# Optimization experiments

Hardware: AMD Instinct MI355X
Metric: run time of the kernel (lower is better)

## Reference

```python
import jax, jax.numpy as jnp
import numpy as np

SR = 8                      # search_range
MO = 2 * SR + 1             # max_offset = 17
NC = MO * MO                # 289 cost-volume channels


def _l2_normalize(x, eps=1e-12):
    # torch F.normalize(p=2, dim=1): x / max(||x||_2, eps)
    n = jnp.sqrt(jnp.sum(x * x, axis=1, keepdims=True))
    return x / jnp.maximum(n, eps)


def _conv2d(x, w, b, pad, groups=1):
    out = jax.lax.conv_general_dilated(
        x, w, window_strides=(1, 1), padding=[(pad, pad), (pad, pad)],
        feature_group_count=groups,
        dimension_numbers=('NCHW', 'OIHW', 'NCHW'))
    return out + b[None, :, None, None]


def _cost_volume(x1, x2, sr, norm_both=False):
    x1 = _l2_normalize(x1)
    if norm_both:
        x2 = _l2_normalize(x2)
    bs, c, h, w = x1.shape
    padded = jnp.pad(x2, ((0, 0), (0, 0), (sr, sr), (sr, sr)))
    mo = 2 * sr + 1
    # offsets in (j outer, i inner) order, matching the original double loop
    jj, ii = jnp.meshgrid(jnp.arange(mo), jnp.arange(mo), indexing='ij')
    offs = jnp.stack([jj.reshape(-1), ii.reshape(-1)], axis=-1)  # [mo^2, 2]

    def step(carry, off):
        sl = jax.lax.dynamic_slice(padded, (0, 0, off[0], off[1]), (bs, c, h, w))
        return carry, jnp.mean(x1 * sl, axis=1)  # [bs, h, w]

    _, cv = jax.lax.scan(step, None, offs)       # [mo^2, bs, h, w]
    cv = jnp.transpose(cv, (1, 0, 2, 3))          # [bs, mo^2, h, w]
    return jax.nn.leaky_relu(cv, 0.1)


def setup_inputs() -> dict:
    key = jax.random.key(0)
    ks = jax.random.split(key, 8)
    bs, c, h, w = 4, 256, 64, 64
    scale = 0.05
    return {
        'f1': jax.random.normal(ks[0], (bs, c, h, w), jnp.float32),
        'f2': jax.random.normal(ks[1], (bs, c, h, w), jnp.float32),
        'att_w': jax.random.normal(ks[2], (NC, 1, 7, 7), jnp.float32) * scale,
        'att_b': jax.random.normal(ks[3], (NC,), jnp.float32) * scale,
        'agg1_w': jax.random.normal(ks[4], (NC // 2, NC, 3, 3), jnp.float32) * scale,
        'agg1_b': jax.random.normal(ks[5], (NC // 2,), jnp.float32) * scale,
        'agg2_w': jax.random.normal(ks[6], (49, NC // 2, 3, 3), jnp.float32) * scale,
        'agg2_b': jax.random.normal(ks[7], (49,), jnp.float32) * scale,
    }


def reference(f1, f2, att_w, att_b, agg1_w, agg1_b, agg2_w, agg2_b):
    match_vol = _cost_volume(f1, f2, SR, norm_both=False)          # [bs,289,h,w]
    att = _conv2d(match_vol, att_w, att_b, pad=3, groups=NC)       # depthwise 7x7
    att_vol = match_vol * att
    h1 = jax.nn.relu(_conv2d(att_vol, agg1_w, agg1_b, pad=1))      # Conv(289->144,3)
    out = jax.nn.relu(_conv2d(h1, agg2_w, agg2_b, pad=1))          # Conv(144->49,3)
    return out
```

## Files before the change

kernel.cpp:

```cpp
#include <hip/hip_runtime.h>
#include <hip/hip_bf16.h>

#define BS   4
#define C    256
#define HW   4096
#define NPIX 16384
#define NCH  289
#define MO   17
#define PH   80
#define PW   80
#define C1   144
#define C2   49
#define ASTR 264
#define ICP  320
#define IC3  192
#define CVP  70
#define CVC  320
#define CH64 72

typedef __bf16  bf16x8 __attribute__((ext_vector_type(8)));
typedef float   f32x4  __attribute__((ext_vector_type(4)));
typedef unsigned short us8 __attribute__((ext_vector_type(8)));

__device__ __forceinline__ void halo_zero_dev(unsigned short* p, int H, int halo,
                                              int Cc, int blk, int t) {
    int W = H;
    int inter = H - 2 * halo;
    int total_pos = H * W - inter * inter;
    int chunks = Cc >> 3;
    size_t tot = (size_t)total_pos * chunks * BS;
    size_t idx = (size_t)blk * 256 + t;
    if (idx >= tot) return;
    int c8 = (int)(idx % chunks);
    size_t r = idx / chunks;
    int pos = (int)(r % total_pos);
    int b = (int)(r / total_pos);
    int h, w;
    int topbot = 2 * halo * W;
    if (pos < halo * W) { h = pos / W; w = pos % W; }
    else if (pos < topbot) { int q = pos - halo * W; h = H - halo + q / W; w = q % W; }
    else {
        int q = pos - topbot;
        int row = q / (2 * halo), off = q % (2 * halo);
        h = halo + row;
        w = (off < halo) ? off : (W - 2 * halo + off);
    }
    us8 z = {0, 0, 0, 0, 0, 0, 0, 0};
    *(us8*)&p[(((size_t)b * H + h) * W + w) * Cc + c8 * 8] = z;
}

__global__ void setup_kernel(unsigned short* __restrict__ x2bf, unsigned short* __restrict__ cvp,
                             unsigned short* __restrict__ avp, unsigned short* __restrict__ h1p,
                             const float* __restrict__ w1, unsigned short* __restrict__ wb1,
                             const float* __restrict__ w2, unsigned short* __restrict__ wb2,
                             const float* __restrict__ att_w, float* __restrict__ wdwp,
                             const float* __restrict__ f1, unsigned short* __restrict__ x1bf,
                             const float* __restrict__ f2) {
    __shared__ float shmem[16 * 257 + 16];
    int blk = blockIdx.x;
    int t = threadIdx.x;
    if (blk < 4030) {
        if (blk < 1152) { halo_zero_dev(x2bf, PH, 8, C, blk, t); return; }
        if (blk < 1655) { halo_zero_dev(cvp, CVP, 3, CVC, blk - 1152, t); return; }
        if (blk < 1818) { halo_zero_dev(avp, 66, 1, ICP, blk - 1655, t); return; }
        if (blk < 1916) { halo_zero_dev(h1p, 66, 1, IC3, blk - 1818, t); return; }
        if (blk < 3536) {
            int idx = (blk - 1916) * 256 + t;
            int tap = idx / (C1 * ICP);
            int r = idx - tap * (C1 * ICP);
            int oc = r / ICP;
            int ic = r - oc * ICP;
            float v = (ic < NCH) ? w1[((size_t)(oc * NCH + ic)) * 9 + tap] : 0.f;
            __hip_bfloat16 hb = __float2bfloat16(v);
            wb1[idx] = *(unsigned short*)&hb;
            return;
        }
        if (blk < 3968) {
            int idx = (blk - 3536) * 256 + t;
            int tap = idx / (64 * IC3);
            int r = idx - tap * (64 * IC3);
            int oc = r / IC3;
            int ic = r - oc * IC3;
            float v = (oc < C2 && ic < C1) ? w2[((size_t)(oc * C1 + ic)) * 9 + tap] : 0.f;
            __hip_bfloat16 hb = __float2bfloat16(v);
            wb2[idx] = *(unsigned short*)&hb;
            return;
        }
        {
            int idx = (blk - 3968) * 256 + t;
            if (idx >= 49 * CVC) return;
            int tap = idx / CVC;
            int ch = idx - tap * CVC;
            wdwp[idx] = (ch < NCH) ? att_w[ch * 49 + tap] : 0.f;
        }
        return;
    }
    if (blk < 5054) {
        float* tileT = shmem;
        float* invS = shmem + 16 * 257;
        int bb = blk - 4030;
        int pblk = bb & 255, b = bb >> 8;
        int p0 = pblk * 16;
        int tx = t & 15, ty = t >> 4;
        const float* s = f1 + (size_t)b * C * HW;
#pragma unroll
        for (int i2 = 0; i2 < 16; ++i2) {
            int c = ty + 16 * i2;
            tileT[tx * 257 + c] = s[(size_t)c * HW + p0 + tx];
        }
        __syncthreads();
        int px = t >> 4;
        int l = t & 15;
        float ssum = 0.f;
#pragma unroll
        for (int j2 = 0; j2 < 16; ++j2) {
            float v = tileT[px * 257 + l + 16 * j2];
            ssum += v * v;
        }
        ssum += __shfl_xor(ssum, 1);
        ssum += __shfl_xor(ssum, 2);
        ssum += __shfl_xor(ssum, 4);
        ssum += __shfl_xor(ssum, 8);
        if (l == 0) invS[px] = 1.0f / fmaxf(sqrtf(ssum), 1e-12f);
        __syncthreads();
#pragma unroll 4
        for (int p = 0; p < 16; ++p) {
            float v = tileT[p * 257 + t] * invS[p];
            __hip_bfloat16 hb = __float2bfloat16(v);
            x1bf[((size_t)b * HW + p0 + p) * C + t] = *(unsigned short*)&hb;
        }
        return;
    }
    {
        float* tile = shmem;
        int bb = blk - 5054;
        int pblk = bb & 127;
        int cblk = (bb >> 7) & 7;
        int b    = bb >> 10;
        int tx = t & 31, ty = t >> 5;
        int c0 = cblk * 32, p0 = pblk * 32;
        const float* s = f2 + (size_t)b * C * HW;
#pragma unroll
        for (int i = 0; i < 4; ++i) {
            int c = c0 + ty + 8 * i;
            tile[(ty + 8 * i) * 33 + tx] = s[(size_t)c * HW + p0 + tx];
        }
        __syncthreads();
#pragma unroll
        for (int i = 0; i < 4; ++i) {
            int p = p0 + ty + 8 * i;
            float v = tile[tx * 33 + ty + 8 * i];
            int c = c0 + tx;
            int h = p >> 6, w = p & 63;
            __hip_bfloat16 hb = __float2bfloat16(v);
            x2bf[(((size_t)b * PH + h + 8) * PW + (w + 8)) * C + c] = *(unsigned short*)&hb;
        }
    }
}

__global__ __launch_bounds__(512, 2)
void cv_mfma_kernel(const unsigned short* __restrict__ x1b,
                    const unsigned short* __restrict__ x2b,
                    unsigned short* __restrict__ cvp) {
    __shared__ __align__(16) unsigned short x2s[2][32 * ASTR];
    int i = blockIdx.x;
    int xcd = i & 7;
    int j = i >> 3;
    int hp = xcd * 2 + (j & 1);
    int jj = j >> 1;
    int wseg = jj & 3;
    int b = jj >> 2;
    int h0 = hp * 4;
    int w0 = wseg * 16;
    int t = threadIdx.x;
    int wave = t >> 6, lane = t & 63;
    int lrow = lane & 15, quad = lane >> 4;
    int row_w = wave >> 1, ct = wave & 1;
    int h = h0 + row_w;
    int col_l = ct * 16 + lrow;

    const unsigned short* x1p = x1b + ((size_t)b * HW + h * 64 + w0) * C;
    bf16x8 a[8];
#pragma unroll
    for (int kk = 0; kk < 8; ++kk)
        a[kk] = *(const bf16x8*)&x1p[(size_t)lrow * C + kk * 32 + quad * 8];

    const unsigned short* x2base = x2b + (size_t)b * PH * PW * C;

    {
        const unsigned short* rowp = x2base + ((size_t)h0 * PW + w0) * C;
#pragma unroll
        for (int s = 0; s < 2; ++s) {
            int v = t + s * 512;
            int col = v >> 5, ch8 = v & 31;
            *(us8*)&x2s[0][col * ASTR + ch8 * 8] = *(const us8*)&rowp[(size_t)col * C + ch8 * 8];
        }
    }
    __syncthreads();

    for (int rr = 0; rr < 20; ++rr) {
        us8 pr[2];
        bool dop = (rr + 1 < 20);
        if (dop) {
            const unsigned short* rowp = x2base + ((size_t)(h0 + rr + 1) * PW + w0) * C;
#pragma unroll
            for (int s = 0; s < 2; ++s) {
                int v = t + s * 512;
                int col = v >> 5, ch8 = v & 31;
                pr[s] = *(const us8*)&rowp[(size_t)col * C + ch8 * 8];
            }
        }

        int dj = rr - row_w;
        if ((unsigned)dj <= 16u) {
            const unsigned short* xs = x2s[rr & 1];
            f32x4 acc = {0.f, 0.f, 0.f, 0.f};
#pragma unroll
            for (int kk = 0; kk < 8; ++kk) {
                bf16x8 bb = *(const bf16x8*)&xs[col_l * ASTR + kk * 32 + quad * 8];
                acc = __builtin_amdgcn_mfma_f32_16x16x32_bf16(a[kk], bb, acc, 0, 0, 0);
            }
#pragma unroll
            for (int r = 0; r < 4; ++r) {
                int px_l = quad * 4 + r;
                int di = col_l - px_l;
                if ((unsigned)di <= 16u) {
                    float v = acc[r] * (1.0f / 256.0f);
                    v = (v > 0.f) ? v : 0.1f * v;
                    __hip_bfloat16 hb = __float2bfloat16(v);
                    cvp[(((size_t)b * CVP + h + 3) * CVP + (w0 + px_l + 3)) * CVC + dj * MO + di] =
                        *(unsigned short*)&hb;
                }
            }
        }

        if (dop) {
            unsigned short* dst = x2s[(rr + 1) & 1];
#pragma unroll
            for (int s = 0; s < 2; ++s) {
                int v = t + s * 512;
                int col = v >> 5, ch8 = v & 31;
                *(us8*)&dst[col * ASTR + ch8 * 8] = pr[s];
            }
            __syncthreads();
        }
    }
}

__global__ __launch_bounds__(256, 4)
void dw_att_tiled(const unsigned short* __restrict__ cvp,
                  const float* __restrict__ wdwp,
                  const float* __restrict__ att_b, unsigned short* __restrict__ av_pad) {
    __shared__ __align__(16) unsigned short actS[14 * 14 * 64];
    __shared__ float wdwS[49 * 64];
    int i = blockIdx.x;
    int ty = i & 7;
    int j = i >> 3;
    int cc = j % 5;
    int rest = j / 5;
    int tx = rest & 7, b = rest >> 3;
    int x0 = tx * 8, y0 = ty * 8;
    int c0 = cc * 64;
    int t = threadIdx.x;

    const unsigned short* cvb = cvp + (((size_t)b * CVP + y0) * CVP + x0) * CVC + c0;
    for (int v = t; v < 14 * 14 * 8; v += 256) {
        int rc = v >> 3, c8v = v & 7;
        int yy = rc / 14, xx = rc - yy * 14;
        *(us8*)&actS[rc * 64 + c8v * 8] =
            *(const us8*)&cvb[((size_t)yy * CVP + xx) * CVC + c8v * 8];
    }
    for (int v = t; v < 49 * 64; v += 256) {
        int tap = v >> 6, ch = v & 63;
        wdwS[v] = wdwp[tap * CVC + c0 + ch];
    }
    __syncthreads();

    int ch_l = t & 63, pgrp = t >> 6;
    int ch = c0 + ch_l;
    float bv = (ch < NCH) ? att_b[ch] : 0.f;
    float acc[16];
#pragma unroll
    for (int ii = 0; ii < 16; ++ii) acc[ii] = bv;

    for (int dy = 0; dy < 7; ++dy) {
        float wreg[7];
#pragma unroll
        for (int dx = 0; dx < 7; ++dx)
            wreg[dx] = wdwS[(dy * 7 + dx) * 64 + ch_l];
#pragma unroll
        for (int py2 = 0; py2 < 2; ++py2) {
            int row = pgrp * 2 + py2 + dy;
            float rowv[14];
#pragma unroll
            for (int xx = 0; xx < 14; ++xx) {
                __bf16 bvv = *(const __bf16*)&actS[(row * 14 + xx) * 64 + ch_l];
                rowv[xx] = (float)bvv;
            }
#pragma unroll
            for (int dx = 0; dx < 7; ++dx)
#pragma unroll
                for (int px = 0; px < 8; ++px)
                    acc[py2 * 8 + px] += rowv[px + dx] * wreg[dx];
        }
    }

    if (ch < NCH) {
#pragma unroll
        for (int ii = 0; ii < 16; ++ii) {
            int py = pgrp * 2 + (ii >> 3), px = ii & 7;
            __bf16 cb = *(const __bf16*)&actS[((py + 3) * 14 + (px + 3)) * 64 + ch_l];
            float c0v = (float)cb;
            __hip_bfloat16 hb = __float2bfloat16(c0v * acc[ii]);
            av_pad[(((size_t)b * 66 + y0 + py + 1) * 66 + (x0 + px + 1)) * ICP + ch] =
                *(unsigned short*)&hb;
        }
    }
}

__global__ void agg1_mfma_kernel(const unsigned short* __restrict__ av_pad,
                                 const unsigned short* __restrict__ wb1,
                                 const float* __restrict__ bias,
                                 unsigned short* __restrict__ h1p) {
    __shared__ __align__(16) unsigned short aS2[2][66 * CH64];
    __shared__ __align__(16) unsigned short bS[2][C1 * CH64];
    int i = blockIdx.x;
    int xcd = i & 7;
    int j = i >> 3;
    int h = xcd * 8 + (j & 7);
    int b = j >> 3;
    int t = threadIdx.x;
    int wave = t >> 6, lane = t & 63;
    int lrow = lane & 15, quad = lane >> 4;
    int ot0 = (wave == 0) ? 0 : (wave * 2 + 1);
    int nt  = (wave == 0) ? 3 : 2;

    f32x4 acc[4][3];
#pragma unroll
    for (int m = 0; m < 4; ++m)
#pragma unroll
        for (int ii = 0; ii < 3; ++ii) acc[m][ii] = (f32x4){0.f, 0.f, 0.f, 0.f};

    const unsigned short* avb = av_pad + (((size_t)b * 66 + h) * 66) * ICP;

    {
        const unsigned short* arow = avb;
#pragma unroll
        for (int s = 0; s < 2; ++s) {
            int v = t + s * 256;
            *(us8*)&aS2[0][(v >> 3) * CH64 + (v & 7) * 8] =
                *(const us8*)&arow[(size_t)(v >> 3) * ICP + (v & 7) * 8];
        }
        if (t < 16) {
            int v = t + 512;
            *(us8*)&aS2[0][(v >> 3) * CH64 + (v & 7) * 8] =
                *(const us8*)&arow[(size_t)(v >> 3) * ICP + (v & 7) * 8];
        }
#pragma unroll
        for (int s = 0; s < 4; ++s) {
            int v = t + s * 256;
            *(us8*)&bS[0][(v >> 3) * CH64 + (v & 7) * 8] =
                *(const us8*)&wb1[(size_t)(v >> 3) * ICP + (v & 7) * 8];
        }
        if (t < 128) {
            int v = t + 1024;
            *(us8*)&bS[0][(v >> 3) * CH64 + (v & 7) * 8] =
                *(const us8*)&wb1[(size_t)(v >> 3) * ICP + (v & 7) * 8];
        }
    }
    __syncthreads();

    for (int k = 0; k < 45; ++k) {
        int rr = k % 15;
        int dx = rr % 3;
        int abuf = (k / 3) & 1, bbuf = k & 1;

        us8 br[5], ar[3];
        int kn = k + 1;
        bool do_b = (kn < 45);
        bool do_a = do_b && (kn % 3 == 0);
        int dyn = kn / 15, rn = kn % 15;
        int ccin = rn / 3, dxn = rn % 3;
        if (do_b) {
            const unsigned short* wt = wb1 + ((size_t)(dyn * 3 + dxn) * C1) * ICP + ccin * 64;
#pragma unroll
            for (int s = 0; s < 4; ++s) {
                int v = t + s * 256;
                br[s] = *(const us8*)&wt[(size_t)(v >> 3) * ICP + (v & 7) * 8];
            }
            if (t < 128) {
                int v = t + 1024;
                br[4] = *(const us8*)&wt[(size_t)(v >> 3) * ICP + (v & 7) * 8];
            }
        }
        if (do_a) {
            const unsigned short* arow = avb + (size_t)dyn * 66 * ICP + ccin * 64;
#pragma unroll
            for (int s = 0; s < 2; ++s) {
                int v = t + s * 256;
                ar[s] = *(const us8*)&arow[(size_t)(v >> 3) * ICP + (v & 7) * 8];
            }
            if (t < 16) {
                int v = t + 512;
                ar[2] = *(const us8*)&arow[(size_t)(v >> 3) * ICP + (v & 7) * 8];
            }
        }

        const unsigned short* aP = aS2[abuf];
        const unsigned short* bP = bS[bbuf];
#pragma unroll
        for (int cc2 = 0; cc2 < 2; ++cc2) {
            bf16x8 bfr[3];
#pragma unroll
            for (int ii = 0; ii < 3; ++ii)
                if (ii < nt)
                    bfr[ii] = *(const bf16x8*)&bP[((ot0 + ii) * 16 + lrow) * CH64 + cc2 * 32 + quad * 8];
#pragma unroll
            for (int m = 0; m < 4; ++m) {
                bf16x8 af = *(const bf16x8*)&aP[(m * 16 + lrow + dx) * CH64 + cc2 * 32 + quad * 8];
#pragma unroll
                for (int ii = 0; ii < 3; ++ii)
                    if (ii < nt)
                        acc[m][ii] = __builtin_amdgcn_mfma_f32_16x16x32_bf16(af, bfr[ii], acc[m][ii], 0, 0, 0);
            }
        }

        if (do_b) {
            unsigned short* dst = bS[bbuf ^ 1];
#pragma unroll
            for (int s = 0; s < 4; ++s) {
                int v = t + s * 256;
                *(us8*)&dst[(v >> 3) * CH64 + (v & 7) * 8] = br[s];
            }
            if (t < 128) {
                int v = t + 1024;
                *(us8*)&dst[(v >> 3) * CH64 + (v & 7) * 8] = br[4];
            }
        }
        if (do_a) {
            unsigned short* dst = aS2[abuf ^ 1];
#pragma unroll
            for (int s = 0; s < 2; ++s) {
                int v = t + s * 256;
                *(us8*)&dst[(v >> 3) * CH64 + (v & 7) * 8] = ar[s];
            }
            if (t < 16) {
                int v = t + 512;
                *(us8*)&dst[(v >> 3) * CH64 + (v & 7) * 8] = ar[2];
            }
        }
        if (do_b) __syncthreads();
    }

    size_t rowbase = ((size_t)b * 66 + h + 1) * 66;
#pragma unroll
    for (int m = 0; m < 4; ++m)
#pragma unroll
        for (int ii = 0; ii < 3; ++ii)
            if (ii < nt) {
                int oc = (ot0 + ii) * 16 + lrow;
                float bv = bias[oc];
#pragma unroll
                for (int r = 0; r < 4; ++r) {
                    int w = m * 16 + quad * 4 + r;
                    float val = fmaxf(acc[m][ii][r] + bv, 0.f);
                    __hip_bfloat16 hb = __float2bfloat16(val);
                    h1p[(rowbase + (w + 1)) * IC3 + oc] = *(unsigned short*)&hb;
                }
            }
}

__global__ void agg2_mfma_kernel(const unsigned short* __restrict__ h1p,
                                 const unsigned short* __restrict__ wb2,
                                 const float* __restrict__ bias, float* __restrict__ out) {
    __shared__ __align__(16) unsigned short aS2[2][66 * CH64];
    __shared__ __align__(16) unsigned short bS2[2][64 * CH64];
    int i = blockIdx.x;
    int xcd = i & 7;
    int j = i >> 3;
    int h = xcd * 8 + (j & 7);
    int b = j >> 3;
    int t = threadIdx.x;
    int wave = t >> 6, lane = t & 63;
    int lrow = lane & 15, quad = lane >> 4;
    int pt = wave;

    f32x4 acc[4];
#pragma unroll
    for (int ot = 0; ot < 4; ++ot) acc[ot] = (f32x4){0.f, 0.f, 0.f, 0.f};

    const unsigned short* h1b = h1p + (((size_t)b * 66 + h) * 66) * IC3;

    {
#pragma unroll
        for (int s = 0; s < 2; ++s) {
            int v = t + s * 256;
            *(us8*)&aS2[0][(v >> 3) * CH64 + (v & 7) * 8] =
                *(const us8*)&h1b[(size_t)(v >> 3) * IC3 + (v & 7) * 8];
        }
        if (t < 16) {
            int v = t + 512;
            *(us8*)&aS2[0][(v >> 3) * CH64 + (v & 7) * 8] =
                *(const us8*)&h1b[(size_t)(v >> 3) * IC3 + (v & 7) * 8];
        }
#pragma unroll
        for (int s = 0; s < 2; ++s) {
            int v = t + s * 256;
            *(us8*)&bS2[0][(v >> 3) * CH64 + (v & 7) * 8] =
                *(const us8*)&wb2[(size_t)(v >> 3) * IC3 + (v & 7) * 8];
        }
    }
    __syncthreads();

    for (int k = 0; k < 27; ++k) {
        int rem = k % 9;
        int dx = rem % 3;
        int abuf = (k / 3) & 1, bbuf = k & 1;

        us8 br[2], ar[3];
        int kn = k + 1;
        bool do_b = (kn < 27);
        bool do_a = do_b && (kn % 3 == 0);
        int dyn = kn / 9, rn = kn % 9;
        int ccn = rn / 3, dxn = rn % 3;
        if (do_b) {
            const unsigned short* wt = wb2 + ((size_t)(dyn * 3 + dxn) * 64) * IC3 + ccn * 64;
#pragma unroll
            for (int s = 0; s < 2; ++s) {
                int v = t + s * 256;
                br[s] = *(const us8*)&wt[(size_t)(v >> 3) * IC3 + (v & 7) * 8];
            }
        }
        if (do_a) {
            const unsigned short* arow = h1b + (size_t)dyn * 66 * IC3 + ccn * 64;
#pragma unroll
            for (int s = 0; s < 2; ++s) {
                int v = t + s * 256;
                ar[s] = *(const us8*)&arow[(size_t)(v >> 3) * IC3 + (v & 7) * 8];
            }
            if (t < 16) {
                int v = t + 512;
                ar[2] = *(const us8*)&arow[(size_t)(v >> 3) * IC3 + (v & 7) * 8];
            }
        }

        const unsigned short* aP = aS2[abuf];
        const unsigned short* bP = bS2[bbuf];
#pragma unroll
        for (int cc2 = 0; cc2 < 2; ++cc2) {
            bf16x8 af = *(const bf16x8*)&aP[(pt * 16 + lrow + dx) * CH64 + cc2 * 32 + quad * 8];
#pragma unroll
            for (int ot = 0; ot < 4; ++ot) {
                bf16x8 bfr = *(const bf16x8*)&bP[(ot * 16 + lrow) * CH64 + cc2 * 32 + quad * 8];
                acc[ot] = __builtin_amdgcn_mfma_f32_16x16x32_bf16(af, bfr, acc[ot], 0, 0, 0);
            }
        }

        if (do_b) {
            unsigned short* dst = bS2[bbuf ^ 1];
#pragma unroll
            for (int s = 0; s < 2; ++s) {
                int v = t + s * 256;
                *(us8*)&dst[(v >> 3) * CH64 + (v & 7) * 8] = br[s];
            }
        }
        if (do_a) {
            unsigned short* dst = aS2[abuf ^ 1];
#pragma unroll
            for (int s = 0; s < 2; ++s) {
                int v = t + s * 256;
                *(us8*)&dst[(v >> 3) * CH64 + (v & 7) * 8] = ar[s];
            }
            if (t < 16) {
                int v = t + 512;
                *(us8*)&dst[(v >> 3) * CH64 + (v & 7) * 8] = ar[2];
            }
        }
        if (do_b) __syncthreads();
    }

#pragma unroll
    for (int ot = 0; ot < 4; ++ot) {
        int o = ot * 16 + lrow;
        if (o < C2) {
            float bv = bias[o];
#pragma unroll
            for (int r = 0; r < 4; ++r) {
                int w = pt * 16 + quad * 4 + r;
                out[((size_t)b * C2 + o) * HW + h * 64 + w] = fmaxf(acc[ot][r] + bv, 0.f);
            }
        }
    }
}

extern "C" void kernel_launch(void* const* d_in, const int* in_sizes, int n_in,
                              void* d_out, int out_size, void* d_ws, size_t ws_size,
                              hipStream_t stream) {
    const float* f1    = (const float*)d_in[0];
    const float* f2    = (const float*)d_in[1];
    const float* att_w = (const float*)d_in[2];
    const float* att_b = (const float*)d_in[3];
    const float* w1    = (const float*)d_in[4];
    const float* b1    = (const float*)d_in[5];
    const float* w2    = (const float*)d_in[6];
    const float* b2    = (const float*)d_in[7];
    float* out = (float*)d_out;

    char* wsb = (char*)d_ws;
    size_t off = 0;
    float* wdwp = (float*)(wsb + off); off += (size_t)49 * CVC * 4;
    off = (off + 15) & ~(size_t)15;
    unsigned short* x1bf = (unsigned short*)(wsb + off); off += (size_t)NPIX * C * 2;
    unsigned short* x2bf = (unsigned short*)(wsb + off); off += (size_t)BS * PH * PW * C * 2;
    unsigned short* cvp  = (unsigned short*)(wsb + off); off += (size_t)BS * CVP * CVP * CVC * 2;
    unsigned short* avp  = (unsigned short*)(wsb + off); off += (size_t)BS * 66 * 66 * ICP * 2;
    unsigned short* wb1  = (unsigned short*)(wsb + off); off += (size_t)9 * C1 * ICP * 2;
    unsigned short* h1p  = (unsigned short*)(wsb + off); off += (size_t)BS * 66 * 66 * IC3 * 2;
    unsigned short* wb2  = (unsigned short*)(wsb + off); off += (size_t)9 * 64 * IC3 * 2;
    if (ws_size < off) return;

    setup_kernel<<<9150, 256, 0, stream>>>(x2bf, cvp, avp, h1p, w1, wb1, w2, wb2,
                                           att_w, wdwp, f1, x1bf, f2);
    cv_mfma_kernel<<<256, 512, 0, stream>>>(x1bf, x2bf, cvp);
    dw_att_tiled<<<1280, 256, 0, stream>>>(cvp, wdwp, att_b, avp);
    agg1_mfma_kernel<<<256, 256, 0, stream>>>(avp, wb1, b1, h1p);
    agg2_mfma_kernel<<<256, 256, 0, stream>>>(h1p, wb2, b2, out);
}
```

Before: 183.3 us.

## Load conv weights straight to registers and pair channels in depthwise attention

In the agg1 and agg2 conv kernels, the weights are no longer staged through double-buffered shared memory. Each lane loads its MFMA B fragments from global memory into registers, prefetching the next tap's fragments while the current tap computes. This cuts the loop down to one barrier per activation-row stage instead of one per tap and frees LDS, which may allow more blocks per CU. The depthwise attention kernel now handles two adjacent channels per thread, using packed 32-bit bf16 loads and stores. The trade-offs are higher register pressure and the risk that weight-fetch latency from global/L2 is exposed.

```diff
diff --git a/kernel.cpp b/kernel.cpp
--- a/kernel.cpp
+++ b/kernel.cpp
@@ -276,44 +276,56 @@
     }
     __syncthreads();
 
-    int ch_l = t & 63, pgrp = t >> 6;
-    int ch = c0 + ch_l;
-    float bv = (ch < NCH) ? att_b[ch] : 0.f;
-    float acc[16];
-#pragma unroll
-    for (int ii = 0; ii < 16; ++ii) acc[ii] = bv;
+    int pr2 = t & 31;
+    int rowg = t >> 5;
+    int chl0 = 2 * pr2;
+    int ch0 = c0 + chl0;
+    float bv0 = (ch0 < NCH) ? att_b[ch0] : 0.f;
+    float bv1 = (ch0 + 1 < NCH) ? att_b[ch0 + 1] : 0.f;
+    float acc0[8], acc1[8];
+#pragma unroll
+    for (int px = 0; px < 8; ++px) { acc0[px] = bv0; acc1[px] = bv1; }
 
     for (int dy = 0; dy < 7; ++dy) {
-        float wreg[7];
+        float w0[7], w1[7];
+#pragma unroll
+        for (int dx = 0; dx < 7; ++dx) {
+            float2 wv = *(const float2*)&wdwS[(dy * 7 + dx) * 64 + chl0];
+            w0[dx] = wv.x; w1[dx] = wv.y;
+        }
+        int row = rowg + dy;
+        float r0[14], r1[14];
+#pragma unroll
+        for (int xx = 0; xx < 14; ++xx) {
+            unsigned u = *(const unsigned*)&actS[(row * 14 + xx) * 64 + chl0];
+            r0[xx] = __uint_as_float(u << 16);
+            r1[xx] = __uint_as_float(u & 0xffff0000u);
+        }
 #pragma unroll
         for (int dx = 0; dx < 7; ++dx)
-            wreg[dx] = wdwS[(dy * 7 + dx) * 64 + ch_l];
-#pragma unroll
-        for (int py2 = 0; py2 < 2; ++py2) {
-            int row = pgrp * 2 + py2 + dy;
-            float rowv[14];
-#pragma unroll
-            for (int xx = 0; xx < 14; ++xx) {
-                __bf16 bvv = *(const __bf16*)&actS[(row * 14 + xx) * 64 + ch_l];
-                rowv[xx] = (float)bvv;
-            }
-#pragma unroll
-            for (int dx = 0; dx < 7; ++dx)
-#pragma unroll
-                for (int px = 0; px < 8; ++px)
-                    acc[py2 * 8 + px] += rowv[px + dx] * wreg[dx];
-        }
-    }
-
-    if (ch < NCH) {
-#pragma unroll
-        for (int ii = 0; ii < 16; ++ii) {
-            int py = pgrp * 2 + (ii >> 3), px = ii & 7;
-            __bf16 cb = *(const __bf16*)&actS[((py + 3) * 14 + (px + 3)) * 64 + ch_l];
-            float c0v = (float)cb;
-            __hip_bfloat16 hb = __float2bfloat16(c0v * acc[ii]);
-            av_pad[(((size_t)b * 66 + y0 + py + 1) * 66 + (x0 + px + 1)) * ICP + ch] =
-                *(unsigned short*)&hb;
+#pragma unroll
+            for (int px = 0; px < 8; ++px) {
+                acc0[px] += r0[px + dx] * w0[dx];
+                acc1[px] += r1[px + dx] * w1[dx];
+            }
+    }
+
+    if (ch0 < NCH) {
+        bool pair = (ch0 + 1 < NCH);
+#pragma unroll
+        for (int px = 0; px < 8; ++px) {
+            unsigned u = *(const unsigned*)&actS[((rowg + 3) * 14 + (px + 3)) * 64 + chl0];
+            float c0v = __uint_as_float(u << 16);
+            float c1v = __uint_as_float(u & 0xffff0000u);
+            __hip_bfloat16 h0 = __float2bfloat16(c0v * acc0[px]);
+            __hip_bfloat16 h1 = __float2bfloat16(c1v * acc1[px]);
+            size_t o = (((size_t)b * 66 + y0 + rowg + 1) * 66 + (x0 + px + 1)) * ICP + ch0;
+            if (pair) {
+                unsigned ov = ((unsigned)*(unsigned short*)&h1 << 16) | (unsigned)*(unsigned short*)&h0;
+                *(unsigned*)&av_pad[o] = ov;
+            } else {
+                av_pad[o] = *(unsigned short*)&h0;
+            }
         }
     }
 }
@@ -323,7 +335,6 @@
                                  const float* __restrict__ bias,
                                  unsigned short* __restrict__ h1p) {
     __shared__ __align__(16) unsigned short aS2[2][66 * CH64];
-    __shared__ __align__(16) unsigned short bS[2][C1 * CH64];
     int i = blockIdx.x;
     int xcd = i & 7;
     int j = i >> 3;
@@ -345,9 +356,10 @@
 
     {
         const unsigned short* arow = avb;
-#pragma unroll
-        for (int s = 0; s < 2; ++s) {
-            int v = t + s * 256;
+        *(us8*)&aS2[0][(t >> 3) * CH64 + (t & 7) * 8] =
+            *(const us8*)&arow[(size_t)(t >> 3) * ICP + (t & 7) * 8];
+        {
+            int v = t + 256;
             *(us8*)&aS2[0][(v >> 3) * CH64 + (v & 7) * 8] =
                 *(const us8*)&arow[(size_t)(v >> 3) * ICP + (v & 7) * 8];
         }
@@ -356,100 +368,85 @@
             *(us8*)&aS2[0][(v >> 3) * CH64 + (v & 7) * 8] =
                 *(const us8*)&arow[(size_t)(v >> 3) * ICP + (v & 7) * 8];
         }
-#pragma unroll
-        for (int s = 0; s < 4; ++s) {
-            int v = t + s * 256;
-            *(us8*)&bS[0][(v >> 3) * CH64 + (v & 7) * 8] =
-                *(const us8*)&wb1[(size_t)(v >> 3) * ICP + (v & 7) * 8];
-        }
-        if (t < 128) {
-            int v = t + 1024;
-            *(us8*)&bS[0][(v >> 3) * CH64 + (v & 7) * 8] =
-                *(const us8*)&wb1[(size_t)(v >> 3) * ICP + (v & 7) * 8];
-        }
-    }
+    }
+    bf16x8 bcur[3][2], bnxt[3][2];
+#pragma unroll
+    for (int ii = 0; ii < 3; ++ii)
+        if (ii < nt)
+#pragma unroll
+            for (int c2 = 0; c2 < 2; ++c2)
+                bcur[ii][c2] = *(const bf16x8*)&wb1[((size_t)((ot0 + ii) * 16 + lrow)) * ICP +
+                                                    c2 * 32 + quad * 8];
     __syncthreads();
 
-    for (int k = 0; k < 45; ++k) {
-        int rr = k % 15;
-        int dx = rr % 3;
-        int abuf = (k / 3) & 1, bbuf = k & 1;
-
-        us8 br[5], ar[3];
-        int kn = k + 1;
-        bool do_b = (kn < 45);
-        bool do_a = do_b && (kn % 3 == 0);
-        int dyn = kn / 15, rn = kn % 15;
-        int ccin = rn / 3, dxn = rn % 3;
-        if (do_b) {
-            const unsigned short* wt = wb1 + ((size_t)(dyn * 3 + dxn) * C1) * ICP + ccin * 64;
-#pragma unroll
-            for (int s = 0; s < 4; ++s) {
-                int v = t + s * 256;
-                br[s] = *(const us8*)&wt[(size_t)(v >> 3) * ICP + (v & 7) * 8];
-            }
-            if (t < 128) {
-                int v = t + 1024;
-                br[4] = *(const us8*)&wt[(size_t)(v >> 3) * ICP + (v & 7) * 8];
-            }
-        }
-        if (do_a) {
-            const unsigned short* arow = avb + (size_t)dyn * 66 * ICP + ccin * 64;
-#pragma unroll
-            for (int s = 0; s < 2; ++s) {
-                int v = t + s * 256;
-                ar[s] = *(const us8*)&arow[(size_t)(v >> 3) * ICP + (v & 7) * 8];
+    for (int p2 = 0; p2 < 15; ++p2) {
+        int dy = p2 / 5, cc = p2 % 5;
+        us8 ar0, ar1, ar2;
+        bool doA = (p2 + 1 < 15);
+        if (doA) {
+            int dyn = (p2 + 1) / 5, ccn = (p2 + 1) % 5;
+            const unsigned short* arow = avb + (size_t)dyn * 66 * ICP + ccn * 64;
+            ar0 = *(const us8*)&arow[(size_t)(t >> 3) * ICP + (t & 7) * 8];
+            {
+                int v = t + 256;
+                ar1 = *(const us8*)&arow[(size_t)(v >> 3) * ICP + (v & 7) * 8];
             }
             if (t < 16) {
                 int v = t + 512;
-                ar[2] = *(const us8*)&arow[(size_t)(v >> 3) * ICP + (v & 7) * 8];
-            }
-        }
-
-        const unsigned short* aP = aS2[abuf];
-        const unsigned short* bP = bS[bbuf];
-#pragma unroll
-        for (int cc2 = 0; cc2 < 2; ++cc2) {
-            bf16x8 bfr[3];
-#pragma unroll
-            for (int ii = 0; ii < 3; ++ii)
-                if (ii < nt)
-                    bfr[ii] = *(const bf16x8*)&bP[((ot0 + ii) * 16 + lrow) * CH64 + cc2 * 32 + quad * 8];
-#pragma unroll
-            for (int m = 0; m < 4; ++m) {
-                bf16x8 af = *(const bf16x8*)&aP[(m * 16 + lrow + dx) * CH64 + cc2 * 32 + quad * 8];
+                ar2 = *(const us8*)&arow[(size_t)(v >> 3) * ICP + (v & 7) * 8];
+            }
+        }
+        const unsigned short* aP = aS2[p2 & 1];
+#pragma unroll
+        for (int dx = 0; dx < 3; ++dx) {
+            bool doB = !(p2 == 14 && dx == 2);
+            if (doB) {
+                int tapn, ccb;
+                if (dx < 2) { tapn = dy * 3 + dx + 1; ccb = cc; }
+                else { tapn = ((p2 + 1) / 5) * 3; ccb = (p2 + 1) % 5; }
+                const unsigned short* wt = wb1 + ((size_t)tapn * C1 + lrow) * ICP +
+                                           ccb * 64 + quad * 8;
 #pragma unroll
                 for (int ii = 0; ii < 3; ++ii)
                     if (ii < nt)
-                        acc[m][ii] = __builtin_amdgcn_mfma_f32_16x16x32_bf16(af, bfr[ii], acc[m][ii], 0, 0, 0);
-            }
-        }
-
-        if (do_b) {
-            unsigned short* dst = bS[bbuf ^ 1];
-#pragma unroll
-            for (int s = 0; s < 4; ++s) {
-                int v = t + s * 256;
-                *(us8*)&dst[(v >> 3) * CH64 + (v & 7) * 8] = br[s];
-            }
-            if (t < 128) {
-                int v = t + 1024;
-                *(us8*)&dst[(v >> 3) * CH64 + (v & 7) * 8] = br[4];
-            }
-        }
-        if (do_a) {
-            unsigned short* dst = aS2[abuf ^ 1];
-#pragma unroll
-            for (int s = 0; s < 2; ++s) {
-                int v = t + s * 256;
-                *(us8*)&dst[(v >> 3) * CH64 + (v & 7) * 8] = ar[s];
+#pragma unroll
+                        for (int c2 = 0; c2 < 2; ++c2)
+                            bnxt[ii][c2] = *(const bf16x8*)&wt[(size_t)((ot0 + ii) * 16) * ICP +
+                                                               c2 * 32];
+            }
+#pragma unroll
+            for (int c2 = 0; c2 < 2; ++c2) {
+#pragma unroll
+                for (int m = 0; m < 4; ++m) {
+                    bf16x8 af = *(const bf16x8*)&aP[(m * 16 + lrow + dx) * CH64 + c2 * 32 + quad * 8];
+#pragma unroll
+                    for (int ii = 0; ii < 3; ++ii)
+                        if (ii < nt)
+                            acc[m][ii] = __builtin_amdgcn_mfma_f32_16x16x32_bf16(af, bcur[ii][c2],
+                                                                                 acc[m][ii], 0, 0, 0);
+                }
+            }
+            if (doB) {
+#pragma unroll
+                for (int ii = 0; ii < 3; ++ii)
+#pragma unroll
+                    for (int c2 = 0; c2 < 2; ++c2)
+                        bcur[ii][c2] = bnxt[ii][c2];
+            }
+        }
+        if (doA) {
+            unsigned short* dst = aS2[(p2 + 1) & 1];
+            *(us8*)&dst[(t >> 3) * CH64 + (t & 7) * 8] = ar0;
+            {
+                int v = t + 256;
+                *(us8*)&dst[(v >> 3) * CH64 + (v & 7) * 8] = ar1;
             }
             if (t < 16) {
                 int v = t + 512;
-                *(us8*)&dst[(v >> 3) * CH64 + (v & 7) * 8] = ar[2];
-            }
-        }
-        if (do_b) __syncthreads();
+                *(us8*)&dst[(v >> 3) * CH64 + (v & 7) * 8] = ar2;
+            }
+            __syncthreads();
+        }
     }
 
     size_t rowbase = ((size_t)b * 66 + h + 1) * 66;
@@ -474,7 +471,6 @@
                                  const unsigned short* __restrict__ wb2,
                                  const float* __restrict__ bias, float* __restrict__ out) {
     __shared__ __align__(16) unsigned short aS2[2][66 * CH64];
-    __shared__ __align__(16) unsigned short bS2[2][64 * CH64];
     int i = blockIdx.x;
     int xcd = i & 7;
     int j = i >> 3;
@@ -492,9 +488,10 @@
     const unsigned short* h1b = h1p + (((size_t)b * 66 + h) * 66) * IC3;
 
     {
-#pragma unroll
-        for (int s = 0; s < 2; ++s) {
-            int v = t + s * 256;
+        *(us8*)&aS2[0][(t >> 3) * CH64 + (t & 7) * 8] =
+            *(const us8*)&h1b[(size_t)(t >> 3) * IC3 + (t & 7) * 8];
+        {
+            int v = t + 256;
             *(us8*)&aS2[0][(v >> 3) * CH64 + (v & 7) * 8] =
                 *(const us8*)&h1b[(size_t)(v >> 3) * IC3 + (v & 7) * 8];
         }
@@ -503,80 +500,78 @@
             *(us8*)&aS2[0][(v >> 3) * CH64 + (v & 7) * 8] =
                 *(const us8*)&h1b[(size_t)(v >> 3) * IC3 + (v & 7) * 8];
         }
-#pragma unroll
-        for (int s = 0; s < 2; ++s) {
-            int v = t + s * 256;
-            *(us8*)&bS2[0][(v >> 3) * CH64 + (v & 7) * 8] =
-                *(const us8*)&wb2[(size_t)(v >> 3) * IC3 + (v & 7) * 8];
-        }
-    }
+    }
+    bf16x8 bcur[4][2], bnxt[4][2];
+#pragma unroll
+    for (int ot = 0; ot < 4; ++ot)
+#pragma unroll
+        for (int c2 = 0; c2 < 2; ++c2)
+            bcur[ot][c2] = *(const bf16x8*)&wb2[((size_t)(ot * 16 + lrow)) * IC3 +
+                                                c2 * 32 + quad * 8];
     __syncthreads();
 
-    for (int k = 0; k < 27; ++k) {
-        int rem = k % 9;
-        int dx = rem % 3;
-        int abuf = (k / 3) & 1, bbuf = k & 1;
-
-        us8 br[2], ar[3];
-        int kn = k + 1;
-        bool do_b = (kn < 27);
-        bool do_a = do_b && (kn % 3 == 0);
-        int dyn = kn / 9, rn = kn % 9;
-        int ccn = rn / 3, dxn = rn % 3;
-        if (do_b) {
-            const unsigned short* wt = wb2 + ((size_t)(dyn * 3 + dxn) * 64) * IC3 + ccn * 64;
-#pragma unroll
-            for (int s = 0; s < 2; ++s) {
-                int v = t + s * 256;
-                br[s] = *(const us8*)&wt[(size_t)(v >> 3) * IC3 + (v & 7) * 8];
-            }
-        }
-        if (do_a) {
+    for (int p2 = 0; p2 < 9; ++p2) {
+        int dy = p2 / 3, cc = p2 % 3;
+        us8 ar0, ar1, ar2;
+        bool doA = (p2 + 1 < 9);
+        if (doA) {
+            int dyn = (p2 + 1) / 3, ccn = (p2 + 1) % 3;
             const unsigned short* arow = h1b + (size_t)dyn * 66 * IC3 + ccn * 64;
-#pragma unroll
-            for (int s = 0; s < 2; ++s) {
-                int v = t + s * 256;
-                ar[s] = *(const us8*)&arow[(size_t)(v >> 3) * IC3 + (v & 7) * 8];
+            ar0 = *(const us8*)&arow[(size_t)(t >> 3) * IC3 + (t & 7) * 8];
+            {
+                int v = t + 256;
+                ar1 = *(const us8*)&arow[(size_t)(v >> 3) * IC3 + (v & 7) * 8];
             }
             if (t < 16) {
                 int v = t + 512;
-                ar[2] = *(const us8*)&arow[(size_t)(v >> 3) * IC3 + (v & 7) * 8];
-            }
-        }
-
-        const unsigned short* aP = aS2[abuf];
-        const unsigned short* bP = bS2[bbuf];
-#pragma unroll
-        for (int cc2 = 0; cc2 < 2; ++cc2) {
-            bf16x8 af = *(const bf16x8*)&aP[(pt * 16 + lrow + dx) * CH64 + cc2 * 32 + quad * 8];
-#pragma unroll
-            for (int ot = 0; ot < 4; ++ot) {
-                bf16x8 bfr = *(const bf16x8*)&bP[(ot * 16 + lrow) * CH64 + cc2 * 32 + quad * 8];
-                acc[ot] = __builtin_amdgcn_mfma_f32_16x16x32_bf16(af, bfr, acc[ot], 0, 0, 0);
-            }
-        }
-
-        if (do_b) {
-            unsigned short* dst = bS2[bbuf ^ 1];
-#pragma unroll
-            for (int s = 0; s < 2; ++s) {
-                int v = t + s * 256;
-                *(us8*)&dst[(v >> 3) * CH64 + (v & 7) * 8] = br[s];
-            }
-        }
-        if (do_a) {
-            unsigned short* dst = aS2[abuf ^ 1];
-#pragma unroll
-            for (int s = 0; s < 2; ++s) {
-                int v = t + s * 256;
-                *(us8*)&dst[(v >> 3) * CH64 + (v & 7) * 8] = ar[s];
+                ar2 = *(const us8*)&arow[(size_t)(v >> 3) * IC3 + (v & 7) * 8];
+            }
+        }
+        const unsigned short* aP = aS2[p2 & 1];
+#pragma unroll
+        for (int dx = 0; dx < 3; ++dx) {
+            bool doB = !(p2 == 8 && dx == 2);
+            if (doB) {
+                int tapn, ccb;
+                if (dx < 2) { tapn = dy * 3 + dx + 1; ccb = cc; }
+                else { tapn = ((p2 + 1) / 3) * 3; ccb = (p2 + 1) % 3; }
+                const unsigned short* wt = wb2 + ((size_t)tapn * 64 + lrow) * IC3 +
+                                           ccb * 64 + quad * 8;
+#pragma unroll
+                for (int ot = 0; ot < 4; ++ot)
+#pragma unroll
+                    for (int c2 = 0; c2 < 2; ++c2)
+                        bnxt[ot][c2] = *(const bf16x8*)&wt[(size_t)(ot * 16) * IC3 + c2 * 32];
+            }
+#pragma unroll
+            for (int c2 = 0; c2 < 2; ++c2) {
+                bf16x8 af = *(const bf16x8*)&aP[(pt * 16 + lrow + dx) * CH64 + c2 * 32 + quad * 8];
+#pragma unroll
+                for (int ot = 0; ot < 4; ++ot)
+                    acc[ot] = __builtin_amdgcn_mfma_f32_16x16x32_bf16(af, bcur[ot][c2],
+                                                                      acc[ot], 0, 0, 0);
+            }
+            if (doB) {
+#pragma unroll
+                for (int ot = 0; ot < 4; ++ot)
+#pragma unroll
+                    for (int c2 = 0; c2 < 2; ++c2)
+                        bcur[ot][c2] = bnxt[ot][c2];
+            }
+        }
+        if (doA) {
+            unsigned short* dst = aS2[(p2 + 1) & 1];
+            *(us8*)&dst[(t >> 3) * CH64 + (t & 7) * 8] = ar0;
+            {
+                int v = t + 256;
+                *(us8*)&dst[(v >> 3) * CH64 + (v & 7) * 8] = ar1;
             }
             if (t < 16) {
                 int v = t + 512;
-                *(us8*)&dst[(v >> 3) * CH64 + (v & 7) * 8] = ar[2];
-            }
-        }
-        if (do_b) __syncthreads();
+                *(us8*)&dst[(v >> 3) * CH64 + (v & 7) * 8] = ar2;
+            }
+            __syncthreads();
+        }
     }
 
 #pragma unroll
```

Result: slower. 205.7 us (+12.2%).

## Split agg convs into half-row blocks and pair channels in depthwise attention

Applied to the files above, without the earlier changes.

The agg1 and agg2 convolution kernels now cover half an output row (32 pixels) per block, which doubles the grid to 512 blocks so more of the device's compute units are busy. Agg2 also redistributes waves across pixel tiles and output-channel groups. Each block re-fetches the full weight tile per k-step for half the pixels, so weight traffic per output roughly doubles. The depthwise attention kernel now handles two adjacent channels and one output row per thread, using 32-bit packed bf16 loads and stores to cut LDS and global memory transactions.

```diff
diff --git a/kernel.cpp b/kernel.cpp
--- a/kernel.cpp
+++ b/kernel.cpp
@@ -276,44 +276,56 @@
     }
     __syncthreads();
 
-    int ch_l = t & 63, pgrp = t >> 6;
-    int ch = c0 + ch_l;
-    float bv = (ch < NCH) ? att_b[ch] : 0.f;
-    float acc[16];
-#pragma unroll
-    for (int ii = 0; ii < 16; ++ii) acc[ii] = bv;
+    int pr2 = t & 31;
+    int rowg = t >> 5;
+    int chl0 = 2 * pr2;
+    int ch0 = c0 + chl0;
+    float bv0 = (ch0 < NCH) ? att_b[ch0] : 0.f;
+    float bv1 = (ch0 + 1 < NCH) ? att_b[ch0 + 1] : 0.f;
+    float acc0[8], acc1[8];
+#pragma unroll
+    for (int px = 0; px < 8; ++px) { acc0[px] = bv0; acc1[px] = bv1; }
 
     for (int dy = 0; dy < 7; ++dy) {
-        float wreg[7];
+        float w0[7], w1[7];
+#pragma unroll
+        for (int dx = 0; dx < 7; ++dx) {
+            float2 wv = *(const float2*)&wdwS[(dy * 7 + dx) * 64 + chl0];
+            w0[dx] = wv.x; w1[dx] = wv.y;
+        }
+        int row = rowg + dy;
+        float r0[14], r1[14];
+#pragma unroll
+        for (int xx = 0; xx < 14; ++xx) {
+            unsigned u = *(const unsigned*)&actS[(row * 14 + xx) * 64 + chl0];
+            r0[xx] = __uint_as_float(u << 16);
+            r1[xx] = __uint_as_float(u & 0xffff0000u);
+        }
 #pragma unroll
         for (int dx = 0; dx < 7; ++dx)
-            wreg[dx] = wdwS[(dy * 7 + dx) * 64 + ch_l];
-#pragma unroll
-        for (int py2 = 0; py2 < 2; ++py2) {
-            int row = pgrp * 2 + py2 + dy;
-            float rowv[14];
-#pragma unroll
-            for (int xx = 0; xx < 14; ++xx) {
-                __bf16 bvv = *(const __bf16*)&actS[(row * 14 + xx) * 64 + ch_l];
-                rowv[xx] = (float)bvv;
-            }
-#pragma unroll
-            for (int dx = 0; dx < 7; ++dx)
-#pragma unroll
-                for (int px = 0; px < 8; ++px)
-                    acc[py2 * 8 + px] += rowv[px + dx] * wreg[dx];
-        }
-    }
-
-    if (ch < NCH) {
-#pragma unroll
-        for (int ii = 0; ii < 16; ++ii) {
-            int py = pgrp * 2 + (ii >> 3), px = ii & 7;
-            __bf16 cb = *(const __bf16*)&actS[((py + 3) * 14 + (px + 3)) * 64 + ch_l];
-            float c0v = (float)cb;
-            __hip_bfloat16 hb = __float2bfloat16(c0v * acc[ii]);
-            av_pad[(((size_t)b * 66 + y0 + py + 1) * 66 + (x0 + px + 1)) * ICP + ch] =
-                *(unsigned short*)&hb;
+#pragma unroll
+            for (int px = 0; px < 8; ++px) {
+                acc0[px] += r0[px + dx] * w0[dx];
+                acc1[px] += r1[px + dx] * w1[dx];
+            }
+    }
+
+    if (ch0 < NCH) {
+        bool pair = (ch0 + 1 < NCH);
+#pragma unroll
+        for (int px = 0; px < 8; ++px) {
+            unsigned u = *(const unsigned*)&actS[((rowg + 3) * 14 + (px + 3)) * 64 + chl0];
+            float c0v = __uint_as_float(u << 16);
+            float c1v = __uint_as_float(u & 0xffff0000u);
+            __hip_bfloat16 h0 = __float2bfloat16(c0v * acc0[px]);
+            __hip_bfloat16 h1 = __float2bfloat16(c1v * acc1[px]);
+            size_t o = (((size_t)b * 66 + y0 + rowg + 1) * 66 + (x0 + px + 1)) * ICP + ch0;
+            if (pair) {
+                unsigned ov = ((unsigned)*(unsigned short*)&h1 << 16) | (unsigned)*(unsigned short*)&h0;
+                *(unsigned*)&av_pad[o] = ov;
+            } else {
+                av_pad[o] = *(unsigned short*)&h0;
+            }
         }
     }
 }
@@ -322,39 +334,36 @@
                                  const unsigned short* __restrict__ wb1,
                                  const float* __restrict__ bias,
                                  unsigned short* __restrict__ h1p) {
-    __shared__ __align__(16) unsigned short aS2[2][66 * CH64];
+    __shared__ __align__(16) unsigned short aS2[2][34 * CH64];
     __shared__ __align__(16) unsigned short bS[2][C1 * CH64];
     int i = blockIdx.x;
     int xcd = i & 7;
     int j = i >> 3;
     int h = xcd * 8 + (j & 7);
-    int b = j >> 3;
+    int wseg = (j >> 3) & 1;
+    int b = j >> 4;
+    int w0 = wseg * 32;
     int t = threadIdx.x;
     int wave = t >> 6, lane = t & 63;
     int lrow = lane & 15, quad = lane >> 4;
     int ot0 = (wave == 0) ? 0 : (wave * 2 + 1);
     int nt  = (wave == 0) ? 3 : 2;
 
-    f32x4 acc[4][3];
-#pragma unroll
-    for (int m = 0; m < 4; ++m)
+    f32x4 acc[2][3];
+#pragma unroll
+    for (int m = 0; m < 2; ++m)
 #pragma unroll
         for (int ii = 0; ii < 3; ++ii) acc[m][ii] = (f32x4){0.f, 0.f, 0.f, 0.f};
 
-    const unsigned short* avb = av_pad + (((size_t)b * 66 + h) * 66) * ICP;
+    const unsigned short* avb = av_pad + (((size_t)b * 66 + h) * 66 + w0) * ICP;
 
     {
-        const unsigned short* arow = avb;
-#pragma unroll
-        for (int s = 0; s < 2; ++s) {
-            int v = t + s * 256;
+        *(us8*)&aS2[0][(t >> 3) * CH64 + (t & 7) * 8] =
+            *(const us8*)&avb[(size_t)(t >> 3) * ICP + (t & 7) * 8];
+        if (t < 16) {
+            int v = t + 256;
             *(us8*)&aS2[0][(v >> 3) * CH64 + (v & 7) * 8] =
-                *(const us8*)&arow[(size_t)(v >> 3) * ICP + (v & 7) * 8];
-        }
-        if (t < 16) {
-            int v = t + 512;
-            *(us8*)&aS2[0][(v >> 3) * CH64 + (v & 7) * 8] =
-                *(const us8*)&arow[(size_t)(v >> 3) * ICP + (v & 7) * 8];
+                *(const us8*)&avb[(size_t)(v >> 3) * ICP + (v & 7) * 8];
         }
 #pragma unroll
         for (int s = 0; s < 4; ++s) {
@@ -371,11 +380,11 @@
     __syncthreads();
 
     for (int k = 0; k < 45; ++k) {
-        int rr = k % 15;
+        int dy = k / 15, rr = k % 15;
         int dx = rr % 3;
         int abuf = (k / 3) & 1, bbuf = k & 1;
 
-        us8 br[5], ar[3];
+        us8 br[5], ar0, ar1;
         int kn = k + 1;
         bool do_b = (kn < 45);
         bool do_a = do_b && (kn % 3 == 0);
@@ -395,14 +404,10 @@
         }
         if (do_a) {
             const unsigned short* arow = avb + (size_t)dyn * 66 * ICP + ccin * 64;
-#pragma unroll
-            for (int s = 0; s < 2; ++s) {
-                int v = t + s * 256;
-                ar[s] = *(const us8*)&arow[(size_t)(v >> 3) * ICP + (v & 7) * 8];
-            }
+            ar0 = *(const us8*)&arow[(size_t)(t >> 3) * ICP + (t & 7) * 8];
             if (t < 16) {
-                int v = t + 512;
-                ar[2] = *(const us8*)&arow[(size_t)(v >> 3) * ICP + (v & 7) * 8];
+                int v = t + 256;
+                ar1 = *(const us8*)&arow[(size_t)(v >> 3) * ICP + (v & 7) * 8];
             }
         }
 
@@ -416,7 +421,7 @@
                 if (ii < nt)
                     bfr[ii] = *(const bf16x8*)&bP[((ot0 + ii) * 16 + lrow) * CH64 + cc2 * 32 + quad * 8];
 #pragma unroll
-            for (int m = 0; m < 4; ++m) {
+            for (int m = 0; m < 2; ++m) {
                 bf16x8 af = *(const bf16x8*)&aP[(m * 16 + lrow + dx) * CH64 + cc2 * 32 + quad * 8];
 #pragma unroll
                 for (int ii = 0; ii < 3; ++ii)
@@ -439,14 +444,10 @@
         }
         if (do_a) {
             unsigned short* dst = aS2[abuf ^ 1];
-#pragma unroll
-            for (int s = 0; s < 2; ++s) {
-                int v = t + s * 256;
-                *(us8*)&dst[(v >> 3) * CH64 + (v & 7) * 8] = ar[s];
-            }
+            *(us8*)&dst[(t >> 3) * CH64 + (t & 7) * 8] = ar0;
             if (t < 16) {
-                int v = t + 512;
-                *(us8*)&dst[(v >> 3) * CH64 + (v & 7) * 8] = ar[2];
+                int v = t + 256;
+                *(us8*)&dst[(v >> 3) * CH64 + (v & 7) * 8] = ar1;
             }
         }
         if (do_b) __syncthreads();
@@ -454,7 +455,7 @@
 
     size_t rowbase = ((size_t)b * 66 + h + 1) * 66;
 #pragma unroll
-    for (int m = 0; m < 4; ++m)
+    for (int m = 0; m < 2; ++m)
 #pragma unroll
         for (int ii = 0; ii < 3; ++ii)
             if (ii < nt) {
@@ -462,10 +463,10 @@
                 float bv = bias[oc];
 #pragma unroll
                 for (int r = 0; r < 4; ++r) {
-                    int w = m * 16 + quad * 4 + r;
+                    int wl = m * 16 + quad * 4 + r;
                     float val = fmaxf(acc[m][ii][r] + bv, 0.f);
                     __hip_bfloat16 hb = __float2bfloat16(val);
-                    h1p[(rowbase + (w + 1)) * IC3 + oc] = *(unsigned short*)&hb;
+                    h1p[(rowbase + (w0 + wl + 1)) * IC3 + oc] = *(unsigned short*)&hb;
                 }
             }
 }
@@ -473,33 +474,32 @@
 __global__ void agg2_mfma_kernel(const unsigned short* __restrict__ h1p,
                                  const unsigned short* __restrict__ wb2,
                                  const float* __restrict__ bias, float* __restrict__ out) {
-    __shared__ __align__(16) unsigned short aS2[2][66 * CH64];
+    __shared__ __align__(16) unsigned short aS2[2][34 * CH64];
     __shared__ __align__(16) unsigned short bS2[2][64 * CH64];
     int i = blockIdx.x;
     int xcd = i & 7;
     int j = i >> 3;
     int h = xcd * 8 + (j & 7);
-    int b = j >> 3;
+    int wseg = (j >> 3) & 1;
+    int b = j >> 4;
+    int w0 = wseg * 32;
     int t = threadIdx.x;
     int wave = t >> 6, lane = t & 63;
     int lrow = lane & 15, quad = lane >> 4;
-    int pt = wave;
-
-    f32x4 acc[4];
-#pragma unroll
-    for (int ot = 0; ot < 4; ++ot) acc[ot] = (f32x4){0.f, 0.f, 0.f, 0.f};
-
-    const unsigned short* h1b = h1p + (((size_t)b * 66 + h) * 66) * IC3;
+    int ptile = wave & 1;
+    int og = wave >> 1;
+
+    f32x4 acc[2];
+#pragma unroll
+    for (int ii = 0; ii < 2; ++ii) acc[ii] = (f32x4){0.f, 0.f, 0.f, 0.f};
+
+    const unsigned short* h1b = h1p + (((size_t)b * 66 + h) * 66 + w0) * IC3;
 
     {
-#pragma unroll
-        for (int s = 0; s < 2; ++s) {
-            int v = t + s * 256;
-            *(us8*)&aS2[0][(v >> 3) * CH64 + (v & 7) * 8] =
-                *(const us8*)&h1b[(size_t)(v >> 3) * IC3 + (v & 7) * 8];
-        }
+        *(us8*)&aS2[0][(t >> 3) * CH64 + (t & 7) * 8] =
+            *(const us8*)&h1b[(size_t)(t >> 3) * IC3 + (t & 7) * 8];
         if (t < 16) {
-            int v = t + 512;
+            int v = t + 256;
             *(us8*)&aS2[0][(v >> 3) * CH64 + (v & 7) * 8] =
                 *(const us8*)&h1b[(size_t)(v >> 3) * IC3 + (v & 7) * 8];
         }
@@ -517,7 +517,7 @@
         int dx = rem % 3;
         int abuf = (k / 3) & 1, bbuf = k & 1;
 
-        us8 br[2], ar[3];
+        us8 br[2], ar0, ar1;
         int kn = k + 1;
         bool do_b = (kn < 27);
         bool do_a = do_b && (kn % 3 == 0);
@@ -533,14 +533,10 @@
         }
         if (do_a) {
             const unsigned short* arow = h1b + (size_t)dyn * 66 * IC3 + ccn * 64;
-#pragma unroll
-            for (int s = 0; s < 2; ++s) {
-                int v = t + s * 256;
-                ar[s] = *(const us8*)&arow[(size_t)(v >> 3) * IC3 + (v & 7) * 8];
-            }
+            ar0 = *(const us8*)&arow[(size_t)(t >> 3) * IC3 + (t & 7) * 8];
             if (t < 16) {
-                int v = t + 512;
-                ar[2] = *(const us8*)&arow[(size_t)(v >> 3) * IC3 + (v & 7) * 8];
+                int v = t + 256;
+                ar1 = *(const us8*)&arow[(size_t)(v >> 3) * IC3 + (v & 7) * 8];
             }
         }
 
@@ -548,11 +544,11 @@
         const unsigned short* bP = bS2[bbuf];
 #pragma unroll
         for (int cc2 = 0; cc2 < 2; ++cc2) {
-            bf16x8 af = *(const bf16x8*)&aP[(pt * 16 + lrow + dx) * CH64 + cc2 * 32 + quad * 8];
-#pragma unroll
-            for (int ot = 0; ot < 4; ++ot) {
-                bf16x8 bfr = *(const bf16x8*)&bP[(ot * 16 + lrow) * CH64 + cc2 * 32 + quad * 8];
-                acc[ot] = __builtin_amdgcn_mfma_f32_16x16x32_bf16(af, bfr, acc[ot], 0, 0, 0);
+            bf16x8 af = *(const bf16x8*)&aP[(ptile * 16 + lrow + dx) * CH64 + cc2 * 32 + quad * 8];
+#pragma unroll
+            for (int ii = 0; ii < 2; ++ii) {
+                bf16x8 bfr = *(const bf16x8*)&bP[((og * 2 + ii) * 16 + lrow) * CH64 + cc2 * 32 + quad * 8];
+                acc[ii] = __builtin_amdgcn_mfma_f32_16x16x32_bf16(af, bfr, acc[ii], 0, 0, 0);
             }
         }
 
@@ -566,28 +562,24 @@
         }
         if (do_a) {
             unsigned short* dst = aS2[abuf ^ 1];
-#pragma unroll
-            for (int s = 0; s < 2; ++s) {
-                int v = t + s * 256;
-                *(us8*)&dst[(v >> 3) * CH64 + (v & 7) * 8] = ar[s];
-            }
+            *(us8*)&dst[(t >> 3) * CH64 + (t & 7) * 8] = ar0;
             if (t < 16) {
-                int v = t + 512;
-                *(us8*)&dst[(v >> 3) * CH64 + (v & 7) * 8] = ar[2];
+                int v = t + 256;
+                *(us8*)&dst[(v >> 3) * CH64 + (v & 7) * 8] = ar1;
             }
         }
         if (do_b) __syncthreads();
     }
 
 #pragma unroll
-    for (int ot = 0; ot < 4; ++ot) {
-        int o = ot * 16 + lrow;
+    for (int ii = 0; ii < 2; ++ii) {
+        int o = (og * 2 + ii) * 16 + lrow;
         if (o < C2) {
             float bv = bias[o];
 #pragma unroll
             for (int r = 0; r < 4; ++r) {
-                int w = pt * 16 + quad * 4 + r;
-                out[((size_t)b * C2 + o) * HW + h * 64 + w] = fmaxf(acc[ot][r] + bv, 0.f);
+                int wl = ptile * 16 + quad * 4 + r;
+                out[((size_t)b * C2 + o) * HW + h * 64 + (w0 + wl)] = fmaxf(acc[ii][r] + bv, 0.f);
             }
         }
     }
@@ -623,6 +615,6 @@
                                            att_w, wdwp, f1, x1bf, f2);
     cv_mfma_kernel<<<256, 512, 0, stream>>>(x1bf, x2bf, cvp);
     dw_att_tiled<<<1280, 256, 0, stream>>>(cvp, wdwp, att_b, avp);
-    agg1_mfma_kernel<<<256, 256, 0, stream>>>(avp, wb1, b1, h1p);
-    agg2_mfma_kernel<<<256, 256, 0, stream>>>(h1p, wb2, b2, out);
+    agg1_mfma_kernel<<<512, 256, 0, stream>>>(avp, wb1, b1, h1p);
+    agg2_mfma_kernel<<<512, 256, 0, stream>>>(h1p, wb2, b2, out);
 }
```

New measurement: 193.1 us. 5.4% more time.
